# Performance work log

Hardware: AMD Instinct MI355X
Metric: run time of the kernel (lower is better)

Reference implementation:

```python
import jax, jax.numpy as jnp
import numpy as np

NEG_BIG = -1e12
ALPHA = 0.2  # LeakyReLU negative slope

def setup_inputs() -> dict:
    key = jax.random.key(0)
    k1, k2, k3, k4, k5 = jax.random.split(key, 5)
    N, F_in, F_out = 8192, 256, 128
    inp = jax.random.normal(k1, (N, F_in), dtype=jnp.float32)
    adj = jax.random.randint(k2, (N, N), 0, 2, dtype=jnp.int32)
    W = jax.random.normal(k3, (F_in, F_out), dtype=jnp.float32) * 0.05
    W_2 = jax.random.normal(k4, (F_in, F_out), dtype=jnp.float32) * 0.05
    W_3 = jax.random.normal(k5, (F_in, F_out), dtype=jnp.float32) * 0.05
    return {"inp": inp, "adj": adj, "W": W, "W_2": W_2, "W_3": W_3}

def reference(inp, adj, W, W_2, W_3):
    # h = inp @ W, h_2 = inp @ W_2  -> scores e = LeakyReLU(h @ h_2^T)  [N, N]
    h = inp @ W
    h_2 = inp @ W_2
    e = jax.nn.leaky_relu(h @ h_2.T, negative_slope=ALPHA)
    # adjacency mask, row softmax (dropout disabled: eval mode)
    attention = jax.nn.softmax(jnp.where(adj > 0, e, NEG_BIG), axis=1)
    h_3 = inp @ W_3
    h_prime = attention @ h_3
    return jax.nn.elu(h_prime)  # concat=True path
```

## Files before the change

### kernel.cpp

```cpp
#include <hip/hip_runtime.h>
#include <hip/hip_fp16.h>

#define N    8192
#define FIN  256
#define FOUT 128
#define BM   64
#define BN   64

typedef _Float16 half8 __attribute__((ext_vector_type(8)));
typedef _Float16 half4v __attribute__((ext_vector_type(4)));
typedef float floatx4 __attribute__((ext_vector_type(4)));

__global__ __launch_bounds__(256)
void maskprep_kernel(const int* __restrict__ adj,
                     unsigned long long* __restrict__ Msk)
{
    const int tid  = threadIdx.x;
    const int wave = tid >> 6;
    const int lane = tid & 63;
    const int task = blockIdx.x * 4 + wave;
    const int row  = task >> 3;
    const int g0   = (task & 7) * 4;
    const int4* base = (const int4*)(adj + (size_t)row * N);
    int4 v[4];
#pragma unroll
    for (int gg = 0; gg < 4; gg++) v[gg] = base[(g0 + gg) * 64 + lane];
#pragma unroll
    for (int gg = 0; gg < 4; gg++) {
        unsigned long long b0 = __ballot(v[gg].x != 0);
        unsigned long long b1 = __ballot(v[gg].y != 0);
        unsigned long long b2 = __ballot(v[gg].z != 0);
        unsigned long long b3 = __ballot(v[gg].w != 0);
        if (lane == 0) {
            unsigned long long* p = &Msk[((size_t)row * 32 + g0 + gg) * 4];
            *(ulonglong2*)&p[0] = make_ulonglong2(b0, b1);
            *(ulonglong2*)&p[2] = make_ulonglong2(b2, b3);
        }
    }
}

__global__ __launch_bounds__(256)
void wprep_kernel(const float* __restrict__ W0,
                  const float* __restrict__ W1,
                  const float* __restrict__ W2,
                  _Float16* __restrict__ Wf)
{
    int idx  = blockIdx.x * 256 + threadIdx.x;
    int lane = idx & 63;
    int frag = idx >> 6;
    int w    = frag >> 6;
    int f    = frag & 63;
    int nt   = f >> 3, kc = f & 7;
    int quad = lane >> 4, lo16 = lane & 15;
    const float* Wp = w == 0 ? W0 : (w == 1 ? W1 : W2);
    half8 v;
#pragma unroll
    for (int jj = 0; jj < 8; jj++)
        v[jj] = (_Float16)Wp[(size_t)(kc * 32 + quad * 8 + jj) * FOUT + nt * 16 + lo16];
    *(half8*)&Wf[(size_t)idx * 8] = v;
}

__global__ __launch_bounds__(256, 2)
void gemm3_kernel(const float* __restrict__ inp,
                  const _Float16* __restrict__ Wf,
                  _Float16* __restrict__ H,
                  _Float16* __restrict__ H2,
                  _Float16* __restrict__ H3T)
{
    const int which = blockIdx.z;
    const int c0    = blockIdx.y * 64;
    const _Float16* Wfw = Wf + (size_t)which * 64 * 64 * 8;
    const int r0 = blockIdx.x * 64;
    const int tid  = threadIdx.x;
    const int wave = tid >> 6;
    const int lane = tid & 63;
    const int lo16 = lane & 15;
    const int quad = lane >> 4;
    const int r = r0 + wave * 16 + lo16;

    half8 a[8];
#pragma unroll
    for (int kc = 0; kc < 8; kc++) {
        const float* p = &inp[(size_t)r * FIN + kc * 32 + quad * 8];
        float4 v0 = *(const float4*)p;
        float4 v1 = *(const float4*)(p + 4);
        a[kc][0] = (_Float16)v0.x; a[kc][1] = (_Float16)v0.y;
        a[kc][2] = (_Float16)v0.z; a[kc][3] = (_Float16)v0.w;
        a[kc][4] = (_Float16)v1.x; a[kc][5] = (_Float16)v1.y;
        a[kc][6] = (_Float16)v1.z; a[kc][7] = (_Float16)v1.w;
    }

    floatx4 acc[4];
#pragma unroll
    for (int i = 0; i < 4; i++) acc[i] = (floatx4){0.f, 0.f, 0.f, 0.f};

#pragma unroll
    for (int kc = 0; kc < 8; kc++)
#pragma unroll
        for (int nt = 0; nt < 4; nt++) {
            int ntg = (c0 >> 4) + nt;
            half8 b = *(const half8*)&Wfw[(((size_t)ntg * 8 + kc) * 64 + lane) * 8];
            acc[nt] = __builtin_amdgcn_mfma_f32_16x16x32_f16(a[kc], b, acc[nt], 0, 0, 0);
        }

    const int arow = wave * 16 + quad * 4;
    if (which < 2) {
        _Float16* outp = which == 0 ? H : H2;
#pragma unroll
        for (int nt = 0; nt < 4; nt++)
#pragma unroll
            for (int rr = 0; rr < 4; rr++)
                outp[(size_t)(r0 + arow + rr) * FOUT + c0 + nt * 16 + lo16] = (_Float16)acc[nt][rr];
    } else {
#pragma unroll
        for (int nt = 0; nt < 4; nt++) {
            half4v v;
#pragma unroll
            for (int rr = 0; rr < 4; rr++) v[rr] = (_Float16)acc[nt][rr];
            *(half4v*)&H3T[(size_t)(c0 + nt * 16 + lo16) * N + r0 + arow] = v;
        }
    }
}

__global__ __launch_bounds__(256)
void repackK_kernel(const _Float16* __restrict__ H2, _Float16* __restrict__ Kf)
{
    int idx  = blockIdx.x * 256 + threadIdx.x;
    int lane = idx & 63;
    int frag = idx >> 6;
    int jb = frag >> 4, f = frag & 15, nt = f >> 2, kc = f & 3;
    int quad = lane >> 4, lo16 = lane & 15;
    half8 v = *(const half8*)&H2[(size_t)(jb * 64 + nt * 16 + lo16) * FOUT + kc * 32 + quad * 8];
    *(half8*)&Kf[(size_t)idx * 8] = v;
}

__global__ __launch_bounds__(256)
void repackV_kernel(const _Float16* __restrict__ H3T, _Float16* __restrict__ Vf)
{
    int idx  = blockIdx.x * 256 + threadIdx.x;
    int lane = idx & 63;
    int frag = idx >> 6;
    int jb = frag >> 4, f = frag & 15, nt = f >> 1, kc = f & 1;
    int quad = lane >> 4, lo16 = lane & 15;
    half8 v = *(const half8*)&H3T[(size_t)(nt * 16 + lo16) * N + jb * 64 + kc * 32 + quad * 8];
    *(half8*)&Vf[(size_t)idx * 8] = v;
}

template<int JS>
__global__ __launch_bounds__(256, 2)
void attn_kernel(const _Float16* __restrict__ Hq,
                 const _Float16* __restrict__ Kf,
                 const _Float16* __restrict__ Vf,
                 const unsigned long long* __restrict__ Msk,
                 float* __restrict__ Opart,
                 float* __restrict__ mpart,
                 float* __restrict__ lpart)
{
    __shared__ _Float16 KV[2][16384];
    __shared__ _Float16 Ps[4][16][BN + 8];

    const int tid  = threadIdx.x;
    const int wave = tid >> 6;
    const int lane = tid & 63;
    const int lo16 = lane & 15;
    const int quad = lane >> 4;
    const int bid  = blockIdx.x;
    const int js   = bid & (JS - 1);
    const int ib   = bid / JS;
    const int i0   = ib * BM;
    const int jbeg = js * (N / JS);
    const int e    = lo16 & 3;
    const int lsh  = lo16 >> 2;
    const int NIT  = (N / JS) / BN;

    half8 q[4];
#pragma unroll
    for (int kc = 0; kc < 4; kc++)
        q[kc] = *(const half8*)&Hq[(size_t)(i0 + wave * 16 + lo16) * FOUT + kc * 32 + quad * 8];

    floatx4 O[8];
#pragma unroll
    for (int i = 0; i < 8; i++) O[i] = (floatx4){0.f, 0.f, 0.f, 0.f};
    float m_r[4], l_r[4];
#pragma unroll
    for (int r = 0; r < 4; r++) { m_r[r] = -1e12f; l_r[r] = 0.f; }

    const int arow = i0 + wave * 16 + quad * 4;
    const int soff = ((size_t)0, (tid * 8));

    {
        const int jb0 = jbeg >> 6;
        const _Float16* gk = Kf + (size_t)jb0 * 8192;
        const _Float16* gv = Vf + (size_t)jb0 * 8192;
#pragma unroll
        for (int r = 0; r < 4; r++) {
            int off = (r * 256 + tid) * 8;
            *(half8*)&KV[0][off]        = *(const half8*)&gk[off];
            *(half8*)&KV[0][8192 + off] = *(const half8*)&gv[off];
        }
        __syncthreads();
    }

    int cur = 0;
    for (int it = 0; it < NIT; it++) {
        const int j0 = jbeg + it * BN;
        const int grp = (j0 >> 8) * 4;
        const int bofs = ((j0 & 255) >> 2) + lsh;

        half8 st[8];
        if (it + 1 < NIT) {
            const int jbn = (j0 + BN) >> 6;
            const _Float16* gk = Kf + (size_t)jbn * 8192;
            const _Float16* gv = Vf + (size_t)jbn * 8192;
#pragma unroll
            for (int r = 0; r < 4; r++) {
                int off = (r * 256 + tid) * 8;
                st[r]     = *(const half8*)&gk[off];
                st[r + 4] = *(const half8*)&gv[off];
            }
        }
        unsigned long long mw[4];
#pragma unroll
        for (int r = 0; r < 4; r++)
            mw[r] = Msk[(size_t)(arow + r) * 128 + e + grp];

        const _Float16* kb = &KV[cur][0];
        const _Float16* vb = &KV[cur][8192];
        floatx4 S[4];
#pragma unroll
        for (int nt = 0; nt < 4; nt++) {
            S[nt] = (floatx4){0.f, 0.f, 0.f, 0.f};
#pragma unroll
            for (int kc = 0; kc < 4; kc++) {
                half8 b = *(const half8*)&kb[((nt * 4 + kc) * 64 + lane) * 8];
                S[nt] = __builtin_amdgcn_mfma_f32_16x16x32_f16(q[kc], b, S[nt], 0, 0, 0);
            }
        }

        float sv[4][4];
#pragma unroll
        for (int nt = 0; nt < 4; nt++)
#pragma unroll
            for (int r = 0; r < 4; r++) {
                float ev = S[nt][r];
                ev = ev > 0.f ? ev : 0.2f * ev;
                sv[nt][r] = ((mw[r] >> (bofs + nt * 4)) & 1ull) ? ev : -1e12f;
            }

        float alpha[4];
#pragma unroll
        for (int r = 0; r < 4; r++) {
            float v = fmaxf(fmaxf(sv[0][r], sv[1][r]), fmaxf(sv[2][r], sv[3][r]));
#pragma unroll
            for (int d = 1; d < 16; d <<= 1)
                v = fmaxf(v, __shfl_xor(v, d));
            float mn = fmaxf(m_r[r], v);
            alpha[r] = __expf(m_r[r] - mn);
            m_r[r] = mn;
        }

        float rs[4] = {0.f, 0.f, 0.f, 0.f};
#pragma unroll
        for (int nt = 0; nt < 4; nt++)
#pragma unroll
            for (int r = 0; r < 4; r++) {
                float p = __expf(sv[nt][r] - m_r[r]);
                rs[r] += p;
                Ps[wave][quad * 4 + r][nt * 16 + lo16] = (_Float16)p;
            }
#pragma unroll
        for (int r = 0; r < 4; r++) {
            float v = rs[r];
#pragma unroll
            for (int d = 1; d < 16; d <<= 1)
                v += __shfl_xor(v, d);
            l_r[r] = l_r[r] * alpha[r] + v;
#pragma unroll
            for (int nt = 0; nt < 8; nt++)
                O[nt][r] *= alpha[r];
        }

        asm volatile("s_waitcnt lgkmcnt(0)" ::: "memory");

#pragma unroll
        for (int kc = 0; kc < BN / 32; kc++) {
            half8 pa = *(const half8*)&Ps[wave][lo16][kc * 32 + quad * 8];
#pragma unroll
            for (int nt = 0; nt < 8; nt++) {
                half8 b = *(const half8*)&vb[((nt * 2 + kc) * 64 + lane) * 8];
                O[nt] = __builtin_amdgcn_mfma_f32_16x16x32_f16(pa, b, O[nt], 0, 0, 0);
            }
        }

        if (it + 1 < NIT) {
            const int nxt = cur ^ 1;
#pragma unroll
            for (int r = 0; r < 4; r++) {
                int off = (r * 256 + tid) * 8;
                *(half8*)&KV[nxt][off]        = st[r];
                *(half8*)&KV[nxt][8192 + off] = st[r + 4];
            }
        }
        __syncthreads();
        cur ^= 1;
    }

#pragma unroll
    for (int nt = 0; nt < 8; nt++)
#pragma unroll
        for (int r = 0; r < 4; r++)
            Opart[((size_t)js * N + arow + r) * FOUT + nt * 16 + lo16] = O[nt][r];
    if (lo16 == 0) {
#pragma unroll
        for (int r = 0; r < 4; r++) {
            mpart[js * N + arow + r] = m_r[r];
            lpart[js * N + arow + r] = l_r[r];
        }
    }
}

template<int JS>
__global__ __launch_bounds__(256)
void combine_kernel(const float* __restrict__ Opart,
                    const float* __restrict__ mpart,
                    const float* __restrict__ lpart,
                    float* __restrict__ out)
{
    int idx = blockIdx.x * 256 + threadIdx.x;
    int i = idx >> 5;
    int c = (idx & 31) << 2;
    float m[JS];
    float M = -3.0e38f;
#pragma unroll
    for (int s = 0; s < JS; s++) { m[s] = mpart[s * N + i]; M = fmaxf(M, m[s]); }
    float w[JS];
    float L = 0.f;
#pragma unroll
    for (int s = 0; s < JS; s++) { w[s] = __expf(m[s] - M); L += lpart[s * N + i] * w[s]; }
    float4 o = {0.f, 0.f, 0.f, 0.f};
#pragma unroll
    for (int s = 0; s < JS; s++) {
        float4 v = *(const float4*)&Opart[((size_t)s * N + i) * FOUT + c];
        o.x += w[s] * v.x; o.y += w[s] * v.y; o.z += w[s] * v.z; o.w += w[s] * v.w;
    }
    float inv = 1.f / L;
    float r0 = o.x * inv, r1 = o.y * inv, r2 = o.z * inv, r3 = o.w * inv;
    float4 res;
    res.x = r0 > 0.f ? r0 : __expf(r0) - 1.f;
    res.y = r1 > 0.f ? r1 : __expf(r1) - 1.f;
    res.z = r2 > 0.f ? r2 : __expf(r2) - 1.f;
    res.w = r3 > 0.f ? r3 : __expf(r3) - 1.f;
    *(float4*)&out[(size_t)i * FOUT + c] = res;
}

extern "C" void kernel_launch(void* const* d_in, const int* in_sizes, int n_in,
                              void* d_out, int out_size, void* d_ws, size_t ws_size,
                              hipStream_t stream) {
    const float* inp = (const float*)d_in[0];
    const int*   adj = (const int*)d_in[1];
    const float* W0  = (const float*)d_in[2];
    const float* W1  = (const float*)d_in[3];
    const float* W2  = (const float*)d_in[4];
    float* out = (float*)d_out;

    char* ws = (char*)d_ws;
    _Float16* H   = (_Float16*)(ws);
    _Float16* H2  = (_Float16*)(ws + (2u << 20));
    _Float16* H3T = (_Float16*)(ws + (4u << 20));
    _Float16* Wf  = (_Float16*)(ws + (6u << 20));
    unsigned long long* Msk = (unsigned long long*)(ws + (7u << 20));
    _Float16* Kf  = (_Float16*)(ws + (15u << 20));
    _Float16* Vf  = (_Float16*)(ws + (17u << 20));
    float* Opart  = (float*)(ws + (19u << 20));

    const size_t need8 = (19ull << 20) + 8ull * N * FOUT * 4 + 2ull * 8 * N * 4;

    maskprep_kernel<<<16384, 256, 0, stream>>>(adj, Msk);
    wprep_kernel<<<48, 256, 0, stream>>>(W0, W1, W2, Wf);
    gemm3_kernel<<<dim3(N / 64, 2, 3), 256, 0, stream>>>(inp, Wf, H, H2, H3T);
    repackK_kernel<<<512, 256, 0, stream>>>(H2, Kf);
    repackV_kernel<<<512, 256, 0, stream>>>(H3T, Vf);

    if (ws_size >= need8) {
        constexpr int JS = 8;
        float* mpart = (float*)(ws + (19u << 20) + (size_t)JS * N * FOUT * 4);
        float* lpart = mpart + (size_t)JS * N;
        attn_kernel<JS><<<(N / BM) * JS, 256, 0, stream>>>(H, Kf, Vf, Msk, Opart, mpart, lpart);
        combine_kernel<JS><<<(N * FOUT / 4) / 256, 256, 0, stream>>>(Opart, mpart, lpart, out);
    } else {
        constexpr int JS = 4;
        float* mpart = (float*)(ws + (19u << 20) + (size_t)JS * N * FOUT * 4);
        float* lpart = mpart + (size_t)JS * N;
        attn_kernel<JS><<<(N / BM) * JS, 256, 0, stream>>>(H, Kf, Vf, Msk, Opart, mpart, lpart);
        combine_kernel<JS><<<(N * FOUT / 4) / 256, 256, 0, stream>>>(Opart, mpart, lpart, out);
    }
}
```

Before: 477.9 us.

## Compute transposed S=K·Q^T in registers to drop LDS P staging, double rows per wave

The attention kernel now computes scores transposed, with K as the A operand and Q as the B operand, so that each lane's score outputs map directly onto the B-operand layout of the P·V MFMA. This removes the per-wave LDS round trip for P. Each wave handles 32 query rows instead of 16, which halves the grid and raises K/V reuse per LDS load. Supporting this, the mask is rebuilt column-major (one 64-bit word per row per 64-column group), K is repacked to match the new lane mapping, and the partial outputs are written transposed, with combine reading them accordingly. The JS=4 fallback for small workspaces is removed, the workspace-size check goes with it, and register pressure rises.

```diff
diff --git a/kernel.cpp b/kernel.cpp
--- a/kernel.cpp
+++ b/kernel.cpp
@@ -4,7 +4,6 @@
 #define N    8192
 #define FIN  256
 #define FOUT 128
-#define BM   64
 #define BN   64
 
 typedef _Float16 half8 __attribute__((ext_vector_type(8)));
@@ -13,29 +12,16 @@
 
 __global__ __launch_bounds__(256)
 void maskprep_kernel(const int* __restrict__ adj,
-                     unsigned long long* __restrict__ Msk)
-{
-    const int tid  = threadIdx.x;
-    const int wave = tid >> 6;
-    const int lane = tid & 63;
-    const int task = blockIdx.x * 4 + wave;
-    const int row  = task >> 3;
-    const int g0   = (task & 7) * 4;
-    const int4* base = (const int4*)(adj + (size_t)row * N);
-    int4 v[4];
-#pragma unroll
-    for (int gg = 0; gg < 4; gg++) v[gg] = base[(g0 + gg) * 64 + lane];
-#pragma unroll
-    for (int gg = 0; gg < 4; gg++) {
-        unsigned long long b0 = __ballot(v[gg].x != 0);
-        unsigned long long b1 = __ballot(v[gg].y != 0);
-        unsigned long long b2 = __ballot(v[gg].z != 0);
-        unsigned long long b3 = __ballot(v[gg].w != 0);
-        if (lane == 0) {
-            unsigned long long* p = &Msk[((size_t)row * 32 + g0 + gg) * 4];
-            *(ulonglong2*)&p[0] = make_ulonglong2(b0, b1);
-            *(ulonglong2*)&p[2] = make_ulonglong2(b2, b3);
-        }
+                     unsigned long long* __restrict__ Msk2)
+{
+    const int wave = threadIdx.x >> 6;
+    const int lane = threadIdx.x & 63;
+    const int row  = blockIdx.x * 4 + wave;
+    const int* base = adj + (size_t)row * N;
+    for (int g = 0; g < 128; g++) {
+        int v = base[g * 64 + lane];
+        unsigned long long b = __ballot(v != 0);
+        if (lane == 0) Msk2[(size_t)g * N + row] = b;
     }
 }
 
@@ -128,9 +114,11 @@
     int idx  = blockIdx.x * 256 + threadIdx.x;
     int lane = idx & 63;
     int frag = idx >> 6;
-    int jb = frag >> 4, f = frag & 15, nt = f >> 2, kc = f & 3;
+    int jb = frag >> 4, f = frag & 15;
+    int c = f >> 3, ntj = (f >> 2) & 1, kc = f & 3;
     int quad = lane >> 4, lo16 = lane & 15;
-    half8 v = *(const half8*)&H2[(size_t)(jb * 64 + nt * 16 + lo16) * FOUT + kc * 32 + quad * 8];
+    int srcrow = jb * 64 + c * 32 + (lo16 >> 2) * 8 + ntj * 4 + (lo16 & 3);
+    half8 v = *(const half8*)&H2[(size_t)srcrow * FOUT + kc * 32 + quad * 8];
     *(half8*)&Kf[(size_t)idx * 8] = v;
 }
 
@@ -151,13 +139,12 @@
 void attn_kernel(const _Float16* __restrict__ Hq,
                  const _Float16* __restrict__ Kf,
                  const _Float16* __restrict__ Vf,
-                 const unsigned long long* __restrict__ Msk,
-                 float* __restrict__ Opart,
+                 const unsigned long long* __restrict__ Msk2,
+                 float* __restrict__ OpartT,
                  float* __restrict__ mpart,
                  float* __restrict__ lpart)
 {
     __shared__ _Float16 KV[2][16384];
-    __shared__ _Float16 Ps[4][16][BN + 8];
 
     const int tid  = threadIdx.x;
     const int wave = tid >> 6;
@@ -167,26 +154,24 @@
     const int bid  = blockIdx.x;
     const int js   = bid & (JS - 1);
     const int ib   = bid / JS;
-    const int i0   = ib * BM;
+    const int i0   = ib * 128;
+    const int iw   = i0 + wave * 32;
     const int jbeg = js * (N / JS);
-    const int e    = lo16 & 3;
-    const int lsh  = lo16 >> 2;
     const int NIT  = (N / JS) / BN;
 
-    half8 q[4];
-#pragma unroll
-    for (int kc = 0; kc < 4; kc++)
-        q[kc] = *(const half8*)&Hq[(size_t)(i0 + wave * 16 + lo16) * FOUT + kc * 32 + quad * 8];
-
-    floatx4 O[8];
-#pragma unroll
-    for (int i = 0; i < 8; i++) O[i] = (floatx4){0.f, 0.f, 0.f, 0.f};
-    float m_r[4], l_r[4];
-#pragma unroll
-    for (int r = 0; r < 4; r++) { m_r[r] = -1e12f; l_r[r] = 0.f; }
-
-    const int arow = i0 + wave * 16 + quad * 4;
-    const int soff = ((size_t)0, (tid * 8));
+    half8 q[2][4];
+#pragma unroll
+    for (int isub = 0; isub < 2; isub++)
+#pragma unroll
+        for (int kc = 0; kc < 4; kc++)
+            q[isub][kc] = *(const half8*)&Hq[(size_t)(iw + isub * 16 + lo16) * FOUT + kc * 32 + quad * 8];
+
+    floatx4 O[8][2];
+#pragma unroll
+    for (int nt = 0; nt < 8; nt++)
+#pragma unroll
+        for (int s = 0; s < 2; s++) O[nt][s] = (floatx4){0.f, 0.f, 0.f, 0.f};
+    float m_s[2] = {-1e12f, -1e12f}, l_s[2] = {0.f, 0.f};
 
     {
         const int jb0 = jbeg >> 6;
@@ -204,8 +189,6 @@
     int cur = 0;
     for (int it = 0; it < NIT; it++) {
         const int j0 = jbeg + it * BN;
-        const int grp = (j0 >> 8) * 4;
-        const int bofs = ((j0 & 255) >> 2) + lsh;
 
         half8 st[8];
         if (it + 1 < NIT) {
@@ -219,78 +202,93 @@
                 st[r + 4] = *(const half8*)&gv[off];
             }
         }
-        unsigned long long mw[4];
-#pragma unroll
-        for (int r = 0; r < 4; r++)
-            mw[r] = Msk[(size_t)(arow + r) * 128 + e + grp];
+        unsigned long long mw[2];
+        mw[0] = Msk2[(size_t)(j0 >> 6) * N + iw + lo16];
+        mw[1] = Msk2[(size_t)(j0 >> 6) * N + iw + 16 + lo16];
 
         const _Float16* kb = &KV[cur][0];
         const _Float16* vb = &KV[cur][8192];
-        floatx4 S[4];
-#pragma unroll
-        for (int nt = 0; nt < 4; nt++) {
-            S[nt] = (floatx4){0.f, 0.f, 0.f, 0.f};
-#pragma unroll
-            for (int kc = 0; kc < 4; kc++) {
-                half8 b = *(const half8*)&kb[((nt * 4 + kc) * 64 + lane) * 8];
-                S[nt] = __builtin_amdgcn_mfma_f32_16x16x32_f16(q[kc], b, S[nt], 0, 0, 0);
-            }
-        }
-
-        float sv[4][4];
-#pragma unroll
-        for (int nt = 0; nt < 4; nt++)
-#pragma unroll
-            for (int r = 0; r < 4; r++) {
-                float ev = S[nt][r];
-                ev = ev > 0.f ? ev : 0.2f * ev;
-                sv[nt][r] = ((mw[r] >> (bofs + nt * 4)) & 1ull) ? ev : -1e12f;
-            }
-
-        float alpha[4];
-#pragma unroll
-        for (int r = 0; r < 4; r++) {
-            float v = fmaxf(fmaxf(sv[0][r], sv[1][r]), fmaxf(sv[2][r], sv[3][r]));
-#pragma unroll
-            for (int d = 1; d < 16; d <<= 1)
-                v = fmaxf(v, __shfl_xor(v, d));
-            float mn = fmaxf(m_r[r], v);
-            alpha[r] = __expf(m_r[r] - mn);
-            m_r[r] = mn;
-        }
-
-        float rs[4] = {0.f, 0.f, 0.f, 0.f};
-#pragma unroll
-        for (int nt = 0; nt < 4; nt++)
-#pragma unroll
-            for (int r = 0; r < 4; r++) {
-                float p = __expf(sv[nt][r] - m_r[r]);
-                rs[r] += p;
-                Ps[wave][quad * 4 + r][nt * 16 + lo16] = (_Float16)p;
-            }
-#pragma unroll
-        for (int r = 0; r < 4; r++) {
-            float v = rs[r];
-#pragma unroll
-            for (int d = 1; d < 16; d <<= 1)
-                v += __shfl_xor(v, d);
-            l_r[r] = l_r[r] * alpha[r] + v;
+
+        floatx4 S[2][2][2];
+#pragma unroll
+        for (int c = 0; c < 2; c++)
+#pragma unroll
+            for (int ntj = 0; ntj < 2; ntj++) {
+                S[c][ntj][0] = (floatx4){0.f, 0.f, 0.f, 0.f};
+                S[c][ntj][1] = (floatx4){0.f, 0.f, 0.f, 0.f};
+#pragma unroll
+                for (int kc = 0; kc < 4; kc++) {
+                    half8 kf = *(const half8*)&kb[(((c * 2 + ntj) * 4 + kc) * 64 + lane) * 8];
+                    S[c][ntj][0] = __builtin_amdgcn_mfma_f32_16x16x32_f16(kf, q[0][kc], S[c][ntj][0], 0, 0, 0);
+                    S[c][ntj][1] = __builtin_amdgcn_mfma_f32_16x16x32_f16(kf, q[1][kc], S[c][ntj][1], 0, 0, 0);
+                }
+            }
+
+        float ev[2][2][2][4];
+#pragma unroll
+        for (int c = 0; c < 2; c++)
+#pragma unroll
+            for (int ntj = 0; ntj < 2; ntj++)
+#pragma unroll
+                for (int s = 0; s < 2; s++)
+#pragma unroll
+                    for (int r = 0; r < 4; r++) {
+                        float e = S[c][ntj][s][r];
+                        ev[c][ntj][s][r] = e > 0.f ? e : 0.2f * e;
+                    }
+
+        float alpha[2];
+#pragma unroll
+        for (int s = 0; s < 2; s++) {
+            float mx = ev[0][0][s][0];
+#pragma unroll
+            for (int c = 0; c < 2; c++)
+#pragma unroll
+                for (int ntj = 0; ntj < 2; ntj++)
+#pragma unroll
+                    for (int r = 0; r < 4; r++)
+                        mx = fmaxf(mx, ev[c][ntj][s][r]);
+            mx = fmaxf(mx, __shfl_xor(mx, 16));
+            mx = fmaxf(mx, __shfl_xor(mx, 32));
+            float mn = fmaxf(m_s[s], mx);
+            alpha[s] = __expf(m_s[s] - mn);
+            m_s[s] = mn;
+        }
+
+        half8 pb[2][2];
+        float sum[2] = {0.f, 0.f};
+#pragma unroll
+        for (int s = 0; s < 2; s++) {
+            unsigned long long mq = mw[s] >> (quad * 8);
+#pragma unroll
+            for (int c = 0; c < 2; c++)
+#pragma unroll
+                for (int ntj = 0; ntj < 2; ntj++)
+#pragma unroll
+                    for (int r = 0; r < 4; r++) {
+                        bool bit = (mq >> (c * 32 + ntj * 4 + r)) & 1ull;
+                        float p = bit ? __expf(ev[c][ntj][s][r] - m_s[s]) : 0.f;
+                        sum[s] += p;
+                        pb[s][c][ntj * 4 + r] = (_Float16)p;
+                    }
+            sum[s] += __shfl_xor(sum[s], 16);
+            sum[s] += __shfl_xor(sum[s], 32);
+            l_s[s] = l_s[s] * alpha[s] + sum[s];
 #pragma unroll
             for (int nt = 0; nt < 8; nt++)
-                O[nt][r] *= alpha[r];
-        }
-
-        asm volatile("s_waitcnt lgkmcnt(0)" ::: "memory");
-
-#pragma unroll
-        for (int kc = 0; kc < BN / 32; kc++) {
-            half8 pa = *(const half8*)&Ps[wave][lo16][kc * 32 + quad * 8];
+#pragma unroll
+                for (int r = 0; r < 4; r++)
+                    O[nt][s][r] *= alpha[s];
+        }
+
+#pragma unroll
+        for (int c = 0; c < 2; c++)
 #pragma unroll
             for (int nt = 0; nt < 8; nt++) {
-                half8 b = *(const half8*)&vb[((nt * 2 + kc) * 64 + lane) * 8];
-                O[nt] = __builtin_amdgcn_mfma_f32_16x16x32_f16(pa, b, O[nt], 0, 0, 0);
-            }
-        }
+                half8 vf = *(const half8*)&vb[((nt * 2 + c) * 64 + lane) * 8];
+                O[nt][0] = __builtin_amdgcn_mfma_f32_16x16x32_f16(vf, pb[0][c], O[nt][0], 0, 0, 0);
+                O[nt][1] = __builtin_amdgcn_mfma_f32_16x16x32_f16(vf, pb[1][c], O[nt][1], 0, 0, 0);
+            }
 
         if (it + 1 < NIT) {
             const int nxt = cur ^ 1;
@@ -308,49 +306,63 @@
 #pragma unroll
     for (int nt = 0; nt < 8; nt++)
 #pragma unroll
-        for (int r = 0; r < 4; r++)
-            Opart[((size_t)js * N + arow + r) * FOUT + nt * 16 + lo16] = O[nt][r];
-    if (lo16 == 0) {
-#pragma unroll
-        for (int r = 0; r < 4; r++) {
-            mpart[js * N + arow + r] = m_r[r];
-            lpart[js * N + arow + r] = l_r[r];
+        for (int s = 0; s < 2; s++)
+#pragma unroll
+            for (int r = 0; r < 4; r++) {
+                int f = nt * 16 + quad * 4 + r;
+                int i = iw + s * 16 + lo16;
+                OpartT[((size_t)js * FOUT + f) * N + i] = O[nt][s][r];
+            }
+    if (quad == 0) {
+#pragma unroll
+        for (int s = 0; s < 2; s++) {
+            mpart[js * N + iw + s * 16 + lo16] = m_s[s];
+            lpart[js * N + iw + s * 16 + lo16] = l_s[s];
         }
     }
 }
 
 template<int JS>
 __global__ __launch_bounds__(256)
-void combine_kernel(const float* __restrict__ Opart,
+void combine_kernel(const float* __restrict__ OpartT,
                     const float* __restrict__ mpart,
                     const float* __restrict__ lpart,
                     float* __restrict__ out)
 {
     int idx = blockIdx.x * 256 + threadIdx.x;
-    int i = idx >> 5;
-    int c = (idx & 31) << 2;
-    float m[JS];
-    float M = -3.0e38f;
-#pragma unroll
-    for (int s = 0; s < JS; s++) { m[s] = mpart[s * N + i]; M = fmaxf(M, m[s]); }
-    float w[JS];
-    float L = 0.f;
-#pragma unroll
-    for (int s = 0; s < JS; s++) { w[s] = __expf(m[s] - M); L += lpart[s * N + i] * w[s]; }
+    int f  = idx >> 11;
+    int i4 = (idx & 2047) << 2;
+
+    float4 M = {-3e38f, -3e38f, -3e38f, -3e38f};
+    float4 m[JS];
+#pragma unroll
+    for (int s = 0; s < JS; s++) {
+        m[s] = *(const float4*)&mpart[s * N + i4];
+        M.x = fmaxf(M.x, m[s].x); M.y = fmaxf(M.y, m[s].y);
+        M.z = fmaxf(M.z, m[s].z); M.w = fmaxf(M.w, m[s].w);
+    }
+    float4 L = {0.f, 0.f, 0.f, 0.f};
+    float4 w[JS];
+#pragma unroll
+    for (int s = 0; s < JS; s++) {
+        float4 l = *(const float4*)&lpart[s * N + i4];
+        w[s].x = __expf(m[s].x - M.x); w[s].y = __expf(m[s].y - M.y);
+        w[s].z = __expf(m[s].z - M.z); w[s].w = __expf(m[s].w - M.w);
+        L.x += l.x * w[s].x; L.y += l.y * w[s].y;
+        L.z += l.z * w[s].z; L.w += l.w * w[s].w;
+    }
     float4 o = {0.f, 0.f, 0.f, 0.f};
 #pragma unroll
     for (int s = 0; s < JS; s++) {
-        float4 v = *(const float4*)&Opart[((size_t)s * N + i) * FOUT + c];
-        o.x += w[s] * v.x; o.y += w[s] * v.y; o.z += w[s] * v.z; o.w += w[s] * v.w;
-    }
-    float inv = 1.f / L;
-    float r0 = o.x * inv, r1 = o.y * inv, r2 = o.z * inv, r3 = o.w * inv;
-    float4 res;
-    res.x = r0 > 0.f ? r0 : __expf(r0) - 1.f;
-    res.y = r1 > 0.f ? r1 : __expf(r1) - 1.f;
-    res.z = r2 > 0.f ? r2 : __expf(r2) - 1.f;
-    res.w = r3 > 0.f ? r3 : __expf(r3) - 1.f;
-    *(float4*)&out[(size_t)i * FOUT + c] = res;
+        float4 v = *(const float4*)&OpartT[((size_t)s * FOUT + f) * N + i4];
+        o.x += w[s].x * v.x; o.y += w[s].y * v.y;
+        o.z += w[s].z * v.z; o.w += w[s].w * v.w;
+    }
+    float r0 = o.x / L.x, r1 = o.y / L.y, r2 = o.z / L.z, r3 = o.w / L.w;
+    out[(size_t)(i4 + 0) * FOUT + f] = r0 > 0.f ? r0 : __expf(r0) - 1.f;
+    out[(size_t)(i4 + 1) * FOUT + f] = r1 > 0.f ? r1 : __expf(r1) - 1.f;
+    out[(size_t)(i4 + 2) * FOUT + f] = r2 > 0.f ? r2 : __expf(r2) - 1.f;
+    out[(size_t)(i4 + 3) * FOUT + f] = r3 > 0.f ? r3 : __expf(r3) - 1.f;
 }
 
 extern "C" void kernel_launch(void* const* d_in, const int* in_sizes, int n_in,
@@ -363,35 +375,24 @@
     const float* W2  = (const float*)d_in[4];
     float* out = (float*)d_out;
 
+    constexpr int JS = 8;
     char* ws = (char*)d_ws;
-    _Float16* H   = (_Float16*)(ws);
-    _Float16* H2  = (_Float16*)(ws + (2u << 20));
-    _Float16* H3T = (_Float16*)(ws + (4u << 20));
-    _Float16* Wf  = (_Float16*)(ws + (6u << 20));
-    unsigned long long* Msk = (unsigned long long*)(ws + (7u << 20));
-    _Float16* Kf  = (_Float16*)(ws + (15u << 20));
-    _Float16* Vf  = (_Float16*)(ws + (17u << 20));
-    float* Opart  = (float*)(ws + (19u << 20));
-
-    const size_t need8 = (19ull << 20) + 8ull * N * FOUT * 4 + 2ull * 8 * N * 4;
-
-    maskprep_kernel<<<16384, 256, 0, stream>>>(adj, Msk);
+    _Float16* H    = (_Float16*)(ws);
+    _Float16* H2   = (_Float16*)(ws + (2u << 20));
+    _Float16* H3T  = (_Float16*)(ws + (4u << 20));
+    _Float16* Wf   = (_Float16*)(ws + (6u << 20));
+    unsigned long long* Msk2 = (unsigned long long*)(ws + (7u << 20));
+    _Float16* Kf   = (_Float16*)(ws + (15u << 20));
+    _Float16* Vf   = (_Float16*)(ws + (17u << 20));
+    float* OpartT  = (float*)(ws + (19u << 20));
+    float* mpart   = (float*)(ws + (51u << 20));
+    float* lpart   = (float*)(ws + (51u << 20) + (size_t)JS * N * sizeof(float));
+
+    maskprep_kernel<<<N / 4, 256, 0, stream>>>(adj, Msk2);
     wprep_kernel<<<48, 256, 0, stream>>>(W0, W1, W2, Wf);
     gemm3_kernel<<<dim3(N / 64, 2, 3), 256, 0, stream>>>(inp, Wf, H, H2, H3T);
     repackK_kernel<<<512, 256, 0, stream>>>(H2, Kf);
     repackV_kernel<<<512, 256, 0, stream>>>(H3T, Vf);
-
-    if (ws_size >= need8) {
-        constexpr int JS = 8;
-        float* mpart = (float*)(ws + (19u << 20) + (size_t)JS * N * FOUT * 4);
-        float* lpart = mpart + (size_t)JS * N;
-        attn_kernel<JS><<<(N / BM) * JS, 256, 0, stream>>>(H, Kf, Vf, Msk, Opart, mpart, lpart);
-        combine_kernel<JS><<<(N * FOUT / 4) / 256, 256, 0, stream>>>(Opart, mpart, lpart, out);
-    } else {
-        constexpr int JS = 4;
-        float* mpart = (float*)(ws + (19u << 20) + (size_t)JS * N * FOUT * 4);
-        float* lpart = mpart + (size_t)JS * N;
-        attn_kernel<JS><<<(N / BM) * JS, 256, 0, stream>>>(H, Kf, Vf, Msk, Opart, mpart, lpart);
-        combine_kernel<JS><<<(N * FOUT / 4) / 256, 256, 0, stream>>>(Opart, mpart, lpart, out);
-    }
-}
+    attn_kernel<JS><<<(N / 128) * JS, 256, 0, stream>>>(H, Kf, Vf, Msk2, OpartT, mpart, lpart);
+    combine_kernel<JS><<<(FOUT * (N / 4)) / 256, 256, 0, stream>>>(OpartT, mpart, lpart, out);
+}
```

New measurement: 486.7 us. Within noise of the previous version (+1.8%).
